# Kernel tuning notes

Measured on AMD Instinct MI355X. Metric: run time of the kernel, lower is better.

Reference implementation:

```python
import jax, jax.numpy as jnp
import numpy as np

LAYER_SIZES = [4096, 8192, 8192, 4096, 1024]
BATCH = 4096
SCARCITY = 0.05


def setup_inputs() -> dict:
    key = jax.random.key(0)
    ks = jax.random.split(key, 5)
    inp = {"x": jax.random.normal(ks[0], (LAYER_SIZES[0], BATCH), dtype=jnp.float32)}
    for i in range(4):
        out_d, in_d = LAYER_SIZES[i + 1], LAYER_SIZES[i]
        # uniform(-0.1, 0.1) mirrors the repo's weight_initialization(a=-0.1, b=0.1)
        inp[f"W{i}"] = jax.random.uniform(ks[i + 1], (out_d, in_d), dtype=jnp.float32,
                                          minval=-0.1, maxval=0.1)
        inp[f"thr{i}"] = jnp.ones((out_d,), dtype=jnp.float32)  # starting_threshold = 1.0
    return inp


def _kwta(x, thr, k):
    # x: [out, batch]; per-column k-winners-take-all on (x - thr)
    act = x - thr[:, None]
    kth = jax.lax.top_k(act.T, k)[0][:, -1]          # [batch] k-th largest per column
    mask = act >= kth[None, :]
    return jnp.where(mask, x, jnp.zeros_like(x))


def reference(x, W0, W1, W2, W3, thr0, thr1, thr2, thr3):
    Ws = [W0, W1, W2, W3]
    thrs = [thr0, thr1, thr2, thr3]
    n_layers = len(Ws)
    for i in range(n_layers):
        x = Ws[i] @ x                                 # [out_i, batch]
        if i < n_layers - 1:
            x = jax.nn.relu(x)
        k = int(SCARCITY * Ws[i].shape[0])
        x = _kwta(x, thrs[i], k)
    return jax.nn.softmax(x, axis=0)                  # output_activation over features
```

## Files before the change

### kernel.cpp

```cpp
#include <hip/hip_runtime.h>

typedef _Float16 f16x8 __attribute__((ext_vector_type(8)));
typedef _Float16 f16x4 __attribute__((ext_vector_type(4)));
typedef float f32x4 __attribute__((ext_vector_type(4)));

#define NB 4096

__device__ __forceinline__ void gload16(const void* g, void* l) {
    __builtin_amdgcn_global_load_lds(
        (const __attribute__((address_space(1))) unsigned int*)g,
        (__attribute__((address_space(3))) unsigned int*)l, 16, 0, 0);
}

__global__ __launch_bounds__(256) void tsplit_kernel(const float* __restrict__ X,
                                                     _Float16* __restrict__ Oh,
                                                     _Float16* __restrict__ Ol) {
    __shared__ float t[64][65];
    const int f0 = blockIdx.x * 64, b0 = blockIdx.y * 64;
    const int tid = threadIdx.x;
    const int jj = tid & 63, i0 = tid >> 6;
#pragma unroll
    for (int p = 0; p < 16; ++p) {
        int i = p * 4 + i0;
        t[i][jj] = X[(size_t)(f0 + i) * NB + b0 + jj];
    }
    __syncthreads();
#pragma unroll
    for (int p = 0; p < 16; ++p) {
        int b = p * 4 + i0;
        float v = t[jj][b];
        size_t idx = (size_t)(b0 + b) * 4096 + f0 + jj;
        _Float16 h = (_Float16)v;
        Oh[idx] = h;
        Ol[idx] = (_Float16)((v - (float)h) * 2048.0f);
    }
}

__global__ __launch_bounds__(256) void splitw_kernel(const float* __restrict__ W,
                                                     _Float16* __restrict__ Wh,
                                                     _Float16* __restrict__ Wl, long n4) {
    long i = (long)blockIdx.x * 256 + threadIdx.x;
    const long stride = (long)gridDim.x * 256;
    for (; i < n4; i += stride) {
        float4 w = ((const float4*)W)[i];
        float vs[4] = {w.x, w.y, w.z, w.w};
        f16x4 h, l;
#pragma unroll
        for (int j = 0; j < 4; ++j) {
            _Float16 hh = (_Float16)vs[j];
            h[j] = hh;
            l[j] = (_Float16)((vs[j] - (float)hh) * 2048.0f);
        }
        ((f16x4*)Wh)[i] = h;
        ((f16x4*)Wl)[i] = l;
    }
}

__global__ __launch_bounds__(256, 2) void gemm3p_kernel(
    const _Float16* __restrict__ Ah, const _Float16* __restrict__ Al,
    const _Float16* __restrict__ Bh, const _Float16* __restrict__ Bl,
    float* __restrict__ C, int K, int M, int do_relu) {
    __shared__ __align__(16) char lds[2][32768];

    const int tid = threadIdx.x;
    const int gx = gridDim.x, gy = gridDim.y;
    int bid = blockIdx.y * gx + blockIdx.x;
    const int SC = gx < 16 ? gx : 16;
    int SR = 512 / SC; if (SR > gy) SR = gy;
    const int W = SC * SR;
    const int nsc = gx / SC;
    const int s = bid / W, w = bid % W;
    const int col0 = ((s % nsc) * SC + (w % SC)) * 128;
    const int row0 = ((s / nsc) * SR + (w / SC)) * 128;

    const int wid = tid >> 6, lane = tid & 63;
    const int wm = wid >> 1, wn = wid & 1;
    const int lr = lane & 15;
    const int rdoff = (((lane >> 4) ^ ((lane >> 1) & 3)) << 4);

    f32x4 acc[4][4] = {};
    f32x4 accx[4][4] = {};

    const int srow = tid >> 2;
    const int scl = (tid & 3) ^ ((tid >> 3) & 3);
    const size_t sk = (size_t)K;
    const _Float16* gA_h = Ah + (size_t)(row0 + srow) * sk + scl * 8;
    const _Float16* gA_h2 = gA_h + 64 * sk;
    const _Float16* gA_l = Al + (size_t)(row0 + srow) * sk + scl * 8;
    const _Float16* gA_l2 = gA_l + 64 * sk;
    const _Float16* gB_h = Bh + (size_t)(col0 + srow) * sk + scl * 8;
    const _Float16* gB_h2 = gB_h + 64 * sk;
    const _Float16* gB_l = Bl + (size_t)(col0 + srow) * sk + scl * 8;
    const _Float16* gB_l2 = gB_l + 64 * sk;
    const int ldsA = tid * 16;

#define SA0(Lb, go) { gload16(gA_h + go, (Lb) + ldsA); gload16(gA_h2 + go, (Lb) + 4096 + ldsA); }
#define SA1(Lb, go) { gload16(gA_l + go, (Lb) + 8192 + ldsA); gload16(gA_l2 + go, (Lb) + 12288 + ldsA); }
#define SB0(Lb, go) { gload16(gB_h + go, (Lb) + 16384 + ldsA); gload16(gB_h2 + go, (Lb) + 20480 + ldsA); }
#define SB1(Lb, go) { gload16(gB_l + go, (Lb) + 24576 + ldsA); gload16(gB_l2 + go, (Lb) + 28672 + ldsA); }

    const int NT = K / 32;
    {
        SA0(lds[0], 0) SA1(lds[0], 0) SB0(lds[0], 0) SB1(lds[0], 0)
    }

    for (int t = 0; t < NT; ++t) {
        asm volatile("s_waitcnt vmcnt(0)" ::: "memory");
        __builtin_amdgcn_s_barrier();
        asm volatile("" ::: "memory");

        const char* Lb = lds[t & 1];
        char* Ls = lds[(t + 1) & 1];
        const bool do_stage = (t + 1 < NT);
        const size_t go = (size_t)(t + 1) * 32;

        f16x8 ah[4], al[4], bh[4], bl[4];
#define READG(i)                                                              \
    {                                                                         \
        const int ra = wm * 64 + (i)*16 + lr;                                 \
        const int rb = wn * 64 + (i)*16 + lr;                                 \
        ah[i] = *(const f16x8*)(Lb + ra * 64 + rdoff);                        \
        al[i] = *(const f16x8*)(Lb + 8192 + ra * 64 + rdoff);                 \
        bh[i] = *(const f16x8*)(Lb + 16384 + rb * 64 + rdoff);                \
        bl[i] = *(const f16x8*)(Lb + 24576 + rb * 64 + rdoff);                \
    }
#define CL(mi, ni)                                                                               \
    {                                                                                            \
        acc[mi][ni] = __builtin_amdgcn_mfma_f32_16x16x32_f16(ah[mi], bh[ni], acc[mi][ni], 0, 0, 0);  \
        accx[mi][ni] = __builtin_amdgcn_mfma_f32_16x16x32_f16(ah[mi], bl[ni], accx[mi][ni], 0, 0, 0); \
        accx[mi][ni] = __builtin_amdgcn_mfma_f32_16x16x32_f16(al[mi], bh[ni], accx[mi][ni], 0, 0, 0); \
    }
        READG(0)
        READG(1)
        if (do_stage) SA0(Ls, go)
        asm volatile("s_waitcnt lgkmcnt(4)" ::: "memory");
        __builtin_amdgcn_sched_barrier(0);
        __builtin_amdgcn_s_setprio(1);
        CL(0, 0)
        __builtin_amdgcn_s_setprio(0);

        READG(2)
        if (do_stage) SA1(Ls, go)
        asm volatile("s_waitcnt lgkmcnt(4)" ::: "memory");
        __builtin_amdgcn_sched_barrier(0);
        __builtin_amdgcn_s_setprio(1);
        CL(0, 1) CL(1, 0) CL(1, 1)
        __builtin_amdgcn_s_setprio(0);

        READG(3)
        if (do_stage) SB0(Ls, go)
        asm volatile("s_waitcnt lgkmcnt(4)" ::: "memory");
        __builtin_amdgcn_sched_barrier(0);
        __builtin_amdgcn_s_setprio(1);
        CL(0, 2) CL(1, 2) CL(2, 0) CL(2, 1) CL(2, 2)
        __builtin_amdgcn_s_setprio(0);

        if (do_stage) SB1(Ls, go)
        asm volatile("s_waitcnt lgkmcnt(0)" ::: "memory");
        __builtin_amdgcn_sched_barrier(0);
        __builtin_amdgcn_s_setprio(1);
        CL(0, 3) CL(1, 3) CL(2, 3) CL(3, 0) CL(3, 1) CL(3, 2) CL(3, 3)
        __builtin_amdgcn_s_setprio(0);
#undef READG
#undef CL
    }
#undef SA0
#undef SA1
#undef SB0
#undef SB1

#pragma unroll
    for (int mi = 0; mi < 4; ++mi)
#pragma unroll
        for (int ni = 0; ni < 4; ++ni) {
            int colx = col0 + wn * 64 + ni * 16 + lr;
            int rowb = row0 + wm * 64 + mi * 16 + ((lane >> 4) << 2);
#pragma unroll
            for (int r = 0; r < 4; ++r) {
                float v = acc[mi][ni][r] + accx[mi][ni][r] * (1.0f / 2048.0f);
                if (do_relu) v = fmaxf(v, 0.0f);
                C[(size_t)(rowb + r) * M + colx] = v;
            }
        }
}

template <int CNT, bool SOFTMAX>
__global__ __launch_bounds__(256) void kwta_kernel(const float* __restrict__ Cin,
                                                   const float* __restrict__ thr,
                                                   _Float16* __restrict__ Oh,
                                                   _Float16* __restrict__ Ol,
                                                   float* __restrict__ outT, int M, int k) {
    const int row = blockIdx.x, tid = threadIdx.x;
    const float* rp = Cin + (size_t)row * M;
    unsigned uv[CNT];
    float xv[CNT];
#pragma unroll
    for (int i = 0; i < CNT; ++i) {
        int col = i * 256 + tid;
        float x = rp[col];
        float a = x - thr[col];
        unsigned b = __float_as_uint(a);
        uv[i] = (b & 0x80000000u) ? ~b : (b | 0x80000000u);
        xv[i] = x;
    }
    __shared__ int hist[256];
    __shared__ unsigned sel_s;
    __shared__ int kk_s;
    unsigned prefix = 0;
    int kk = k;
#pragma unroll
    for (int pass = 0; pass < 4; ++pass) {
        const int shift = 24 - pass * 8;
        hist[tid] = 0;
        __syncthreads();
#pragma unroll
        for (int i = 0; i < CNT; ++i) {
            bool ok = (pass == 0) || ((uv[i] >> (shift + 8)) == prefix);
            if (ok) atomicAdd(&hist[(uv[i] >> shift) & 255], 1);
        }
        __syncthreads();
        for (int off = 1; off < 256; off <<= 1) {
            int v = hist[tid] + ((tid + off < 256) ? hist[tid + off] : 0);
            __syncthreads();
            hist[tid] = v;
            __syncthreads();
        }
        if (hist[tid] >= kk && (tid == 255 || hist[tid + 1] < kk)) {
            sel_s = (unsigned)tid;
            kk_s = kk - ((tid == 255) ? 0 : hist[tid + 1]);
        }
        __syncthreads();
        prefix = (prefix << 8) | sel_s;
        kk = kk_s;
        __syncthreads();
    }
    const unsigned kth = prefix;
    if (!SOFTMAX) {
#pragma unroll
        for (int i = 0; i < CNT; ++i) {
            int col = i * 256 + tid;
            float v = (uv[i] >= kth) ? xv[i] : 0.0f;
            size_t idx = (size_t)row * M + col;
            _Float16 h = (_Float16)v;
            Oh[idx] = h;
            Ol[idx] = (_Float16)((v - (float)h) * 2048.0f);
        }
    } else {
        float vals[CNT];
        float m = -3.4e38f;
#pragma unroll
        for (int i = 0; i < CNT; ++i) {
            float v = (uv[i] >= kth) ? xv[i] : 0.0f;
            vals[i] = v;
            m = fmaxf(m, v);
        }
        for (int off = 32; off; off >>= 1) m = fmaxf(m, __shfl_xor(m, off));
        __shared__ float redm[4];
        if ((tid & 63) == 0) redm[tid >> 6] = m;
        __syncthreads();
        m = fmaxf(fmaxf(redm[0], redm[1]), fmaxf(redm[2], redm[3]));
        float s = 0.0f, e[CNT];
#pragma unroll
        for (int i = 0; i < CNT; ++i) {
            e[i] = expf(vals[i] - m);
            s += e[i];
        }
        for (int off = 32; off; off >>= 1) s += __shfl_xor(s, off);
        __shared__ float reds[4];
        if ((tid & 63) == 0) reds[tid >> 6] = s;
        __syncthreads();
        s = reds[0] + reds[1] + reds[2] + reds[3];
        float inv = 1.0f / s;
#pragma unroll
        for (int i = 0; i < CNT; ++i)
            outT[(size_t)(i * 256 + tid) * NB + row] = e[i] * inv;
    }
}

extern "C" void kernel_launch(void* const* d_in, const int* in_sizes, int n_in,
                              void* d_out, int out_size, void* d_ws, size_t ws_size,
                              hipStream_t stream) {
    const float* x = (const float*)d_in[0];
    const float* W0 = (const float*)d_in[1];
    const float* thr0 = (const float*)d_in[2];
    const float* W1 = (const float*)d_in[3];
    const float* thr1 = (const float*)d_in[4];
    const float* W2 = (const float*)d_in[5];
    const float* thr2 = (const float*)d_in[6];
    const float* W3 = (const float*)d_in[7];
    const float* thr3 = (const float*)d_in[8];
    float* out = (float*)d_out;

    char* ws = (char*)d_ws;
    size_t off = 0;
    auto alloc = [&](size_t bytes) {
        void* p = ws + off;
        off += (bytes + 255) & ~(size_t)255;
        return p;
    };
    _Float16* Wh = (_Float16*)alloc((size_t)8192 * 8192 * 2);
    _Float16* Wl = (_Float16*)alloc((size_t)8192 * 8192 * 2);
    _Float16* Xh = (_Float16*)alloc((size_t)4096 * 8192 * 2);
    _Float16* Xl = (_Float16*)alloc((size_t)4096 * 8192 * 2);
    _Float16* Yh = (_Float16*)alloc((size_t)4096 * 8192 * 2);
    _Float16* Yl = (_Float16*)alloc((size_t)4096 * 8192 * 2);
    float* C32 = (float*)alloc((size_t)4096 * 8192 * 4);

    tsplit_kernel<<<dim3(64, 64), 256, 0, stream>>>(x, Xh, Xl);

    splitw_kernel<<<4096, 256, 0, stream>>>(W0, Wh, Wl, (long)8192 * 4096 / 4);
    gemm3p_kernel<<<dim3(8192 / 128, NB / 128), 256, 0, stream>>>(Xh, Xl, Wh, Wl, C32, 4096, 8192, 1);
    kwta_kernel<32, false><<<NB, 256, 0, stream>>>(C32, thr0, Yh, Yl, nullptr, 8192, 409);

    splitw_kernel<<<4096, 256, 0, stream>>>(W1, Wh, Wl, (long)8192 * 8192 / 4);
    gemm3p_kernel<<<dim3(8192 / 128, NB / 128), 256, 0, stream>>>(Yh, Yl, Wh, Wl, C32, 8192, 8192, 1);
    kwta_kernel<32, false><<<NB, 256, 0, stream>>>(C32, thr1, Xh, Xl, nullptr, 8192, 409);

    splitw_kernel<<<4096, 256, 0, stream>>>(W2, Wh, Wl, (long)4096 * 8192 / 4);
    gemm3p_kernel<<<dim3(4096 / 128, NB / 128), 256, 0, stream>>>(Xh, Xl, Wh, Wl, C32, 8192, 4096, 1);
    kwta_kernel<16, false><<<NB, 256, 0, stream>>>(C32, thr2, Yh, Yl, nullptr, 4096, 204);

    splitw_kernel<<<4096, 256, 0, stream>>>(W3, Wh, Wl, (long)1024 * 4096 / 4);
    gemm3p_kernel<<<dim3(1024 / 128, NB / 128), 256, 0, stream>>>(Yh, Yl, Wh, Wl, C32, 4096, 1024, 0);
    kwta_kernel<4, true><<<NB, 256, 0, stream>>>(C32, thr3, nullptr, nullptr, out, 1024, 51);
}
```

Measured before the change: 3.362 ms.

## Issue all next-tile loads upfront and shrink block swizzle group

Moves all eight global-to-LDS prefetch loads for the next K tile to the top of the loop iteration instead of interleaving them between the LDS reads and MFMA groups. The aim is to give the global loads the whole iteration to complete. The block-swizzle supergroup is also halved (8 columns by up to 32 rows instead of 16 by 32), which changes L2 reuse locality. Issuing all loads at once may contend with the LDS reads, and the smaller group could lower cache reuse.

Result: slower. 4.538 ms (+35.0%).

```diff
diff --git a/kernel.cpp b/kernel.cpp
--- a/kernel.cpp
+++ b/kernel.cpp
@@ -65,8 +65,8 @@
     const int tid = threadIdx.x;
     const int gx = gridDim.x, gy = gridDim.y;
     int bid = blockIdx.y * gx + blockIdx.x;
-    const int SC = gx < 16 ? gx : 16;
-    int SR = 512 / SC; if (SR > gy) SR = gy;
+    const int SC = gx < 8 ? gx : 8;
+    int SR = 256 / SC; if (SR > gy) SR = gy;
     const int W = SC * SR;
     const int nsc = gx / SC;
     const int s = bid / W, w = bid % W;
@@ -94,15 +94,20 @@
     const _Float16* gB_l2 = gB_l + 64 * sk;
     const int ldsA = tid * 16;
 
-#define SA0(Lb, go) { gload16(gA_h + go, (Lb) + ldsA); gload16(gA_h2 + go, (Lb) + 4096 + ldsA); }
-#define SA1(Lb, go) { gload16(gA_l + go, (Lb) + 8192 + ldsA); gload16(gA_l2 + go, (Lb) + 12288 + ldsA); }
-#define SB0(Lb, go) { gload16(gB_h + go, (Lb) + 16384 + ldsA); gload16(gB_h2 + go, (Lb) + 20480 + ldsA); }
-#define SB1(Lb, go) { gload16(gB_l + go, (Lb) + 24576 + ldsA); gload16(gB_l2 + go, (Lb) + 28672 + ldsA); }
+#define STAGE8(Lb, go)                                          \
+    {                                                           \
+        gload16(gA_h + go, (Lb) + ldsA);                        \
+        gload16(gA_h2 + go, (Lb) + 4096 + ldsA);                \
+        gload16(gA_l + go, (Lb) + 8192 + ldsA);                 \
+        gload16(gA_l2 + go, (Lb) + 12288 + ldsA);               \
+        gload16(gB_h + go, (Lb) + 16384 + ldsA);                \
+        gload16(gB_h2 + go, (Lb) + 20480 + ldsA);               \
+        gload16(gB_l + go, (Lb) + 24576 + ldsA);                \
+        gload16(gB_l2 + go, (Lb) + 28672 + ldsA);               \
+    }
 
     const int NT = K / 32;
-    {
-        SA0(lds[0], 0) SA1(lds[0], 0) SB0(lds[0], 0) SB1(lds[0], 0)
-    }
+    STAGE8(lds[0], 0)
 
     for (int t = 0; t < NT; ++t) {
         asm volatile("s_waitcnt vmcnt(0)" ::: "memory");
@@ -111,8 +116,10 @@
 
         const char* Lb = lds[t & 1];
         char* Ls = lds[(t + 1) & 1];
-        const bool do_stage = (t + 1 < NT);
-        const size_t go = (size_t)(t + 1) * 32;
+        if (t + 1 < NT) {
+            const size_t go = (size_t)(t + 1) * 32;
+            STAGE8(Ls, go)
+        }
 
         f16x8 ah[4], al[4], bh[4], bl[4];
 #define READG(i)                                                              \
@@ -132,7 +139,6 @@
     }
         READG(0)
         READG(1)
-        if (do_stage) SA0(Ls, go)
         asm volatile("s_waitcnt lgkmcnt(4)" ::: "memory");
         __builtin_amdgcn_sched_barrier(0);
         __builtin_amdgcn_s_setprio(1);
@@ -140,7 +146,6 @@
         __builtin_amdgcn_s_setprio(0);
 
         READG(2)
-        if (do_stage) SA1(Ls, go)
         asm volatile("s_waitcnt lgkmcnt(4)" ::: "memory");
         __builtin_amdgcn_sched_barrier(0);
         __builtin_amdgcn_s_setprio(1);
@@ -148,14 +153,12 @@
         __builtin_amdgcn_s_setprio(0);
 
         READG(3)
-        if (do_stage) SB0(Ls, go)
         asm volatile("s_waitcnt lgkmcnt(4)" ::: "memory");
         __builtin_amdgcn_sched_barrier(0);
         __builtin_amdgcn_s_setprio(1);
         CL(0, 2) CL(1, 2) CL(2, 0) CL(2, 1) CL(2, 2)
         __builtin_amdgcn_s_setprio(0);
 
-        if (do_stage) SB1(Ls, go)
         asm volatile("s_waitcnt lgkmcnt(0)" ::: "memory");
         __builtin_amdgcn_sched_barrier(0);
         __builtin_amdgcn_s_setprio(1);
@@ -164,10 +167,7 @@
 #undef READG
 #undef CL
     }
-#undef SA0
-#undef SA1
-#undef SB0
-#undef SB1
+#undef STAGE8
 
 #pragma unroll
     for (int mi = 0; mi < 4; ++mi)
```

## Load B operand fragments directly from global into registers, bypassing LDS

Applied to the files above, without the earlier changes.

The GEMM now stages only the A operand (high and low halves) through double-buffered LDS. Each wave loads its B fragments straight from global memory into registers with inline global_load_dwordx4, and the waits on vmcnt are interleaved per MFMA group. This halves LDS footprint and LDS traffic, which may allow more occupancy and fewer LDS bank stalls. In exchange B tiles are no longer shared across waves, so global/L2 traffic for B doubles (each wn pair reloads them), and the uncoalesced per-lane row loads add latency exposure. The last iteration also restages a redundant A tile instead of skipping it.

Measured after the change: 5.489 ms. 1.63x slower.

```diff
diff --git a/kernel.cpp b/kernel.cpp
--- a/kernel.cpp
+++ b/kernel.cpp
@@ -56,11 +56,11 @@
     }
 }
 
-__global__ __launch_bounds__(256, 2) void gemm3p_kernel(
-    const _Float16* __restrict__ Ah, const _Float16* __restrict__ Al,
-    const _Float16* __restrict__ Bh, const _Float16* __restrict__ Bl,
+__global__ __launch_bounds__(256, 2) void gemm3d_kernel(
+    const _Float16* __restrict__ Ah_, const _Float16* __restrict__ Al_,
+    const _Float16* __restrict__ Bh_, const _Float16* __restrict__ Bl_,
     float* __restrict__ C, int K, int M, int do_relu) {
-    __shared__ __align__(16) char lds[2][32768];
+    __shared__ __align__(16) char lds[2][16384];
 
     const int tid = threadIdx.x;
     const int gx = gridDim.x, gy = gridDim.y;
@@ -76,7 +76,8 @@
     const int wid = tid >> 6, lane = tid & 63;
     const int wm = wid >> 1, wn = wid & 1;
     const int lr = lane & 15;
-    const int rdoff = (((lane >> 4) ^ ((lane >> 1) & 3)) << 4);
+    const int q = (lane >> 4) & 3;
+    const int rdoff = ((q ^ ((lane >> 1) & 3)) << 4);
 
     f32x4 acc[4][4] = {};
     f32x4 accx[4][4] = {};
@@ -84,25 +85,31 @@
     const int srow = tid >> 2;
     const int scl = (tid & 3) ^ ((tid >> 3) & 3);
     const size_t sk = (size_t)K;
-    const _Float16* gA_h = Ah + (size_t)(row0 + srow) * sk + scl * 8;
+    const _Float16* gA_h = Ah_ + (size_t)(row0 + srow) * sk + scl * 8;
     const _Float16* gA_h2 = gA_h + 64 * sk;
-    const _Float16* gA_l = Al + (size_t)(row0 + srow) * sk + scl * 8;
+    const _Float16* gA_l = Al_ + (size_t)(row0 + srow) * sk + scl * 8;
     const _Float16* gA_l2 = gA_l + 64 * sk;
-    const _Float16* gB_h = Bh + (size_t)(col0 + srow) * sk + scl * 8;
-    const _Float16* gB_h2 = gB_h + 64 * sk;
-    const _Float16* gB_l = Bl + (size_t)(col0 + srow) * sk + scl * 8;
-    const _Float16* gB_l2 = gB_l + 64 * sk;
     const int ldsA = tid * 16;
 
-#define SA0(Lb, go) { gload16(gA_h + go, (Lb) + ldsA); gload16(gA_h2 + go, (Lb) + 4096 + ldsA); }
-#define SA1(Lb, go) { gload16(gA_l + go, (Lb) + 8192 + ldsA); gload16(gA_l2 + go, (Lb) + 12288 + ldsA); }
-#define SB0(Lb, go) { gload16(gB_h + go, (Lb) + 16384 + ldsA); gload16(gB_h2 + go, (Lb) + 20480 + ldsA); }
-#define SB1(Lb, go) { gload16(gB_l + go, (Lb) + 24576 + ldsA); gload16(gB_l2 + go, (Lb) + 28672 + ldsA); }
+    unsigned long long pBh[4], pBl[4];
+#pragma unroll
+    for (int ni = 0; ni < 4; ++ni) {
+        size_t rb = (size_t)(col0 + wn * 64 + ni * 16 + lr);
+        pBh[ni] = (unsigned long long)(Bh_ + rb * sk + q * 8);
+        pBl[ni] = (unsigned long long)(Bl_ + rb * sk + q * 8);
+    }
+
+#define GLOADB(d, p) asm volatile("global_load_dwordx4 %0, %1, off" : "=v"(d) : "v"(p) : "memory")
+#define STAGE4(Lb, go)                                  \
+    {                                                   \
+        gload16(gA_h + go, (Lb) + ldsA);                \
+        gload16(gA_h2 + go, (Lb) + 4096 + ldsA);        \
+        gload16(gA_l + go, (Lb) + 8192 + ldsA);         \
+        gload16(gA_l2 + go, (Lb) + 12288 + ldsA);       \
+    }
 
     const int NT = K / 32;
-    {
-        SA0(lds[0], 0) SA1(lds[0], 0) SB0(lds[0], 0) SB1(lds[0], 0)
-    }
+    STAGE4(lds[0], 0)
 
     for (int t = 0; t < NT; ++t) {
         asm volatile("s_waitcnt vmcnt(0)" ::: "memory");
@@ -111,63 +118,65 @@
 
         const char* Lb = lds[t & 1];
         char* Ls = lds[(t + 1) & 1];
-        const bool do_stage = (t + 1 < NT);
-        const size_t go = (size_t)(t + 1) * 32;
-
-        f16x8 ah[4], al[4], bh[4], bl[4];
-#define READG(i)                                                              \
-    {                                                                         \
-        const int ra = wm * 64 + (i)*16 + lr;                                 \
-        const int rb = wn * 64 + (i)*16 + lr;                                 \
-        ah[i] = *(const f16x8*)(Lb + ra * 64 + rdoff);                        \
-        al[i] = *(const f16x8*)(Lb + 8192 + ra * 64 + rdoff);                 \
-        bh[i] = *(const f16x8*)(Lb + 16384 + rb * 64 + rdoff);                \
-        bl[i] = *(const f16x8*)(Lb + 24576 + rb * 64 + rdoff);                \
-    }
-#define CL(mi, ni)                                                                               \
-    {                                                                                            \
+
+        f16x8 bh[4], bl[4];
+        GLOADB(bh[0], pBh[0]); GLOADB(bl[0], pBl[0]);
+        GLOADB(bh[1], pBh[1]); GLOADB(bl[1], pBl[1]);
+        GLOADB(bh[2], pBh[2]); GLOADB(bl[2], pBl[2]);
+        GLOADB(bh[3], pBh[3]); GLOADB(bl[3], pBl[3]);
+#pragma unroll
+        for (int ni = 0; ni < 4; ++ni) { pBh[ni] += 64; pBl[ni] += 64; }
+
+        f16x8 ah[4], al[4];
+#define READA(i)                                                      \
+    {                                                                 \
+        const int ra = wm * 64 + (i)*16 + lr;                         \
+        ah[i] = *(const f16x8*)(Lb + ra * 64 + rdoff);                \
+        al[i] = *(const f16x8*)(Lb + 8192 + ra * 64 + rdoff);         \
+    }
+#define CL(mi, ni)                                                                                   \
+    {                                                                                                \
         acc[mi][ni] = __builtin_amdgcn_mfma_f32_16x16x32_f16(ah[mi], bh[ni], acc[mi][ni], 0, 0, 0);  \
         accx[mi][ni] = __builtin_amdgcn_mfma_f32_16x16x32_f16(ah[mi], bl[ni], accx[mi][ni], 0, 0, 0); \
         accx[mi][ni] = __builtin_amdgcn_mfma_f32_16x16x32_f16(al[mi], bh[ni], accx[mi][ni], 0, 0, 0); \
     }
-        READG(0)
-        READG(1)
-        if (do_stage) SA0(Ls, go)
-        asm volatile("s_waitcnt lgkmcnt(4)" ::: "memory");
+        READA(0)
+        READA(1)
+        {
+            const size_t go = (size_t)((t + 1 < NT) ? t + 1 : t) * 32;
+            STAGE4(Ls, go)
+        }
+        asm volatile("s_waitcnt vmcnt(10) lgkmcnt(2)" ::: "memory");
         __builtin_amdgcn_sched_barrier(0);
         __builtin_amdgcn_s_setprio(1);
         CL(0, 0)
         __builtin_amdgcn_s_setprio(0);
 
-        READG(2)
-        if (do_stage) SA1(Ls, go)
-        asm volatile("s_waitcnt lgkmcnt(4)" ::: "memory");
+        READA(2)
+        asm volatile("s_waitcnt vmcnt(8) lgkmcnt(2)" ::: "memory");
         __builtin_amdgcn_sched_barrier(0);
         __builtin_amdgcn_s_setprio(1);
         CL(0, 1) CL(1, 0) CL(1, 1)
         __builtin_amdgcn_s_setprio(0);
 
-        READG(3)
-        if (do_stage) SB0(Ls, go)
-        asm volatile("s_waitcnt lgkmcnt(4)" ::: "memory");
+        READA(3)
+        asm volatile("s_waitcnt vmcnt(6) lgkmcnt(2)" ::: "memory");
         __builtin_amdgcn_sched_barrier(0);
         __builtin_amdgcn_s_setprio(1);
         CL(0, 2) CL(1, 2) CL(2, 0) CL(2, 1) CL(2, 2)
         __builtin_amdgcn_s_setprio(0);
 
-        if (do_stage) SB1(Ls, go)
-        asm volatile("s_waitcnt lgkmcnt(0)" ::: "memory");
+        asm volatile("s_waitcnt vmcnt(4) lgkmcnt(0)" ::: "memory");
         __builtin_amdgcn_sched_barrier(0);
         __builtin_amdgcn_s_setprio(1);
         CL(0, 3) CL(1, 3) CL(2, 3) CL(3, 0) CL(3, 1) CL(3, 2) CL(3, 3)
         __builtin_amdgcn_s_setprio(0);
-#undef READG
+#undef READA
 #undef CL
     }
-#undef SA0
-#undef SA1
-#undef SB0
-#undef SB1
+    asm volatile("s_waitcnt vmcnt(0)" ::: "memory");
+#undef STAGE4
+#undef GLOADB
 
 #pragma unroll
     for (int mi = 0; mi < 4; ++mi)
@@ -309,18 +318,18 @@
     tsplit_kernel<<<dim3(64, 64), 256, 0, stream>>>(x, Xh, Xl);
 
     splitw_kernel<<<4096, 256, 0, stream>>>(W0, Wh, Wl, (long)8192 * 4096 / 4);
-    gemm3p_kernel<<<dim3(8192 / 128, NB / 128), 256, 0, stream>>>(Xh, Xl, Wh, Wl, C32, 4096, 8192, 1);
+    gemm3d_kernel<<<dim3(8192 / 128, NB / 128), 256, 0, stream>>>(Xh, Xl, Wh, Wl, C32, 4096, 8192, 1);
     kwta_kernel<32, false><<<NB, 256, 0, stream>>>(C32, thr0, Yh, Yl, nullptr, 8192, 409);
 
     splitw_kernel<<<4096, 256, 0, stream>>>(W1, Wh, Wl, (long)8192 * 8192 / 4);
-    gemm3p_kernel<<<dim3(8192 / 128, NB / 128), 256, 0, stream>>>(Yh, Yl, Wh, Wl, C32, 8192, 8192, 1);
+    gemm3d_kernel<<<dim3(8192 / 128, NB / 128), 256, 0, stream>>>(Yh, Yl, Wh, Wl, C32, 8192, 8192, 1);
     kwta_kernel<32, false><<<NB, 256, 0, stream>>>(C32, thr1, Xh, Xl, nullptr, 8192, 409);
 
     splitw_kernel<<<4096, 256, 0, stream>>>(W2, Wh, Wl, (long)4096 * 8192 / 4);
-    gemm3p_kernel<<<dim3(4096 / 128, NB / 128), 256, 0, stream>>>(Xh, Xl, Wh, Wl, C32, 8192, 4096, 1);
+    gemm3d_kernel<<<dim3(4096 / 128, NB / 128), 256, 0, stream>>>(Xh, Xl, Wh, Wl, C32, 8192, 4096, 1);
     kwta_kernel<16, false><<<NB, 256, 0, stream>>>(C32, thr2, Yh, Yl, nullptr, 4096, 204);
 
     splitw_kernel<<<4096, 256, 0, stream>>>(W3, Wh, Wl, (long)1024 * 4096 / 4);
-    gemm3p_kernel<<<dim3(1024 / 128, NB / 128), 256, 0, stream>>>(Yh, Yl, Wh, Wl, C32, 4096, 1024, 0);
+    gemm3d_kernel<<<dim3(1024 / 128, NB / 128), 256, 0, stream>>>(Yh, Yl, Wh, Wl, C32, 4096, 1024, 0);
     kwta_kernel<4, true><<<NB, 256, 0, stream>>>(C32, thr3, nullptr, nullptr, out, 1024, 51);
 }
```
